# Optimization experiments

Hardware: AMD Instinct MI355X
Metric: run time of the kernel (lower is better)

Reference implementation:

```python
import jax, jax.numpy as jnp
import numpy as np

H, D, TS, A, R, TR = 256, 2, 32, 4, 16, 8  # h_size, max_output_degree, t_size, n_aggr, rank, t_rank
BS = 16384


def setup_inputs() -> dict:
    key = jax.random.key(0)
    ks = jax.random.split(key, 9)
    return {
        "neighbour_h": jax.random.normal(ks[0], (BS, D, H), jnp.float32),
        "type_embs": jax.random.normal(ks[1], (BS, TS), jnp.float32),
        # per-child input projections U: (max_output_degree, n_aggr, h_size, rank)
        "U": jax.random.normal(ks[2], (D, A, H, R), jnp.float32) * 0.05,
        "b": jax.random.normal(ks[3], (D, A, 1, R), jnp.float32) * 0.05,
        # type projection
        "U_type": jax.random.normal(ks[4], (TS, A * TR), jnp.float32) * 0.05,
        "b_type": jax.random.normal(ks[5], (1, A * TR), jnp.float32) * 0.05,
        # stacked augmented core tensors T_list: (n_aggr, t_rank+1, rank+1, rank+1, rank)
        "T": jax.random.normal(ks[6], (A, TR + 1, R + 1, R + 1, R), jnp.float32) * 0.02,
        # output projection
        "U_output": jax.random.normal(ks[7], (A, R, H), jnp.float32) * 0.05,
        "b_output": jax.random.normal(ks[8], (A, 1, H), jnp.float32) * 0.05,
    }


def _aug(x):
    # append a constant-1 feature along the last dim: (bs, a, d) -> (bs, a, d+1)
    bs, a, _ = x.shape
    return jnp.concatenate([x, jnp.ones((bs, a, 1), x.dtype)], axis=-1)


def reference(neighbour_h, type_embs, U, b, U_type, b_type, T, U_output, b_output):
    # child projections: (bs, n_ch, n_aggr, rank)
    ch = jnp.einsum('bch,cahr->bcar', neighbour_h, U) + b[:, :, 0, :]
    # type projection: (bs, n_aggr, t_rank)
    tp = (type_embs @ U_type + b_type).reshape(-1, A, TR)
    # augmented (homogeneous) inputs
    h0 = _aug(tp)         # (bs, a, TR+1)
    h1 = _aug(ch[:, 0])   # (bs, a, R+1)
    h2 = _aug(ch[:, 1])   # (bs, a, R+1)
    # sequential multilinear (Tucker/HOSVD) contraction with the core tensor,
    # vectorized over batch and aggregators (original loops over n_aggr)
    r = jnp.einsum('bap,apqrs->baqrs', h0, T)
    r = jnp.einsum('baq,baqrs->bars', h1, r)
    g = jnp.einsum('bar,bars->bas', h2, r)            # (bs, a, R)
    out = jnp.einsum('bar,arh->bah', g, U_output) + b_output[:, 0, :]
    return out.reshape(neighbour_h.shape[0], -1)      # (bs, n_aggr*h_size)
```

## Files before the change

### kernel.cpp

```cpp
#include <hip/hip_runtime.h>

#define NTHR 512
#define TB 32

typedef __attribute__((ext_vector_type(8))) short bf16x8;
typedef __attribute__((ext_vector_type(16))) float f32x16;
typedef float4 f4;
typedef unsigned short u16;

__device__ __forceinline__ u16 f2b(float x) {
  union { float f; unsigned u; } v; v.f = x;
  unsigned r = (v.u + 0x7fffu + ((v.u >> 16) & 1u)) >> 16;
  return (u16)r;
}
__device__ __forceinline__ float b2f(u16 u) {
  union { unsigned u; float f; } v; v.u = ((unsigned)u) << 16;
  return v.f;
}
__device__ __forceinline__ unsigned pack2(float a, float b) {
  return (unsigned)f2b(a) | ((unsigned)f2b(b) << 16);
}
__device__ __forceinline__ unsigned cvtpk(float lo, float hi) {
  unsigned r;
  asm("v_cvt_pk_bf16_f32 %0, %1, %2" : "=v"(r) : "v"(lo), "v"(hi));
  return r;
}

#define MFMA32(A, B, C) __builtin_amdgcn_mfma_f32_32x32x16_bf16(A, B, C, 0, 0, 0)

extern "C" __global__ void hosvd_prep(const float* __restrict__ U,
                                      const float* __restrict__ T,
                                      const float* __restrict__ UO,
                                      unsigned* __restrict__ ws32) {
  int id = blockIdx.x * 256 + threadIdx.x;
  if (id < 102400) {
    int j2 = id & 3, frag = id >> 2;
    int l = frag & 63, f2 = frag >> 6;
    int nt = f2 % 5, aks = f2 / 5;
    int ks = aks % 20, a = aks / 20;
    int n = nt * 32 + (l & 31);
    int p = n >> 4, s = n & 15;
    float v[2];
    #pragma unroll
    for (int j = 0; j < 2; ++j) {
      int kp = ks * 16 + (l >> 5) * 8 + j2 * 2 + j;
      int q = (unsigned)kp / 18u, r = kp - q * 18;
      float x = 0.f;
      if (p <= 8 && q <= 16 && r <= 16)
        x = T[(((a * 9 + p) * 17 + q) * 17 + r) * 16 + s];
      v[j] = x;
    }
    ws32[id] = pack2(v[0], v[1]);
  } else if (id < 118784) {
    int rel = id - 102400;
    int j2 = rel & 3, frag = rel >> 2;
    int l = frag & 63, f2 = frag >> 6;
    int nt = f2 & 1, ks = (f2 >> 1) & 15, c = f2 >> 5;
    int n = nt * 32 + (l & 31);
    int a = n >> 4, rr = n & 15;
    int k = ks * 16 + (l >> 5) * 8 + j2 * 2;
    float v0 = U[((c * 4 + a) * 256 + k + 0) * 16 + rr];
    float v1 = U[((c * 4 + a) * 256 + k + 1) * 16 + rr];
    ws32[id] = pack2(v0, v1);
  } else if (id < 126976) {
    int rel = id - 118784;
    int j2 = rel & 3, frag = rel >> 2;
    int l = frag & 63, f2 = frag >> 6;
    int ht = f2 & 7, a = f2 >> 3;
    int h = ht * 32 + (l & 31);
    int k = (l >> 5) * 8 + j2 * 2;
    float v0 = UO[(a * 16 + k + 0) * 256 + h];
    float v1 = UO[(a * 16 + k + 1) * 256 + h];
    ws32[id] = pack2(v0, v1);
  }
}

extern "C" __global__ __launch_bounds__(NTHR, 4)
void hosvd_main(const float* __restrict__ nh, const float* __restrict__ te,
                const float* __restrict__ bw, const float* __restrict__ Ut,
                const float* __restrict__ bt, const float* __restrict__ bO,
                const u16* __restrict__ BTf, const u16* __restrict__ UcTf,
                const u16* __restrict__ UOTf, float* __restrict__ out) {
  __shared__ __align__(16) u16   s_u[20800];
  __shared__ __align__(16) u16   s_ch[TB * 164];
  __shared__ __align__(16) float s_tpt[36 * 32];

  const int t = threadIdx.x;
  const int ib0 = blockIdx.x * TB;
  const int w = t >> 6, l = t & 63;
  const int l31 = l & 31, hi = l >> 5;

  float* UtL = (float*)&s_u[16640];
  float* teL = (float*)&s_u[18688];
  float* s_redf = (float*)s_u;

  if (t < 256) {
    const int row = t >> 3, cc = (t >> 2) & 1, aa = t & 3;
    *(uint2*)&s_ch[row * 164 + cc * 80 + aa * 20 + 16] = make_uint2(0x3F80u, 0u);
  }
  if (t < 128) {
    const int aa = t >> 5, row = t & 31;
    s_tpt[(aa * 9 + 8) * 32 + row] = 1.0f;
  }

  if (t < 256) {
    const int row = t >> 3, k4 = t & 7;
    f4 v = *(const f4*)&te[(size_t)(ib0 + row) * 32 + k4 * 4];
    float* d = &teL[row * 33 + k4 * 4];
    d[0] = v.x; d[1] = v.y; d[2] = v.z; d[3] = v.w;
  } else {
    const int j = t - 256;
    *(f4*)&UtL[j * 4] = *(const f4*)&Ut[j * 4];
  }
  for (int lp = t; lp < 4096; lp += NTHR) {
    const int row = lp >> 7, rem = lp & 127;
    const int c = rem >> 6, k0 = (rem & 63) * 4;
    f4 v = *(const f4*)&nh[((size_t)(ib0 + row) * 2 + c) * 256 + k0];
    *(uint2*)&s_u[row * 520 + c * 256 + k0] =
        make_uint2(cvtpk(v.x, v.y), cvtpk(v.z, v.w));
  }
  __syncthreads();

  if (w < 4) {
    const int c = w & 1, nt2 = w >> 1;
    f32x16 accC = {0.f, 0.f, 0.f, 0.f, 0.f, 0.f, 0.f, 0.f,
                   0.f, 0.f, 0.f, 0.f, 0.f, 0.f, 0.f, 0.f};
    #pragma unroll
    for (int ks = 0; ks < 16; ++ks) {
      bf16x8 Av = *(const bf16x8*)&s_u[l31 * 520 + c * 256 + ks * 16 + hi * 8];
      bf16x8 Bv = *(const bf16x8*)
          &UcTf[(size_t)(((c * 16 + ks) * 2 + nt2) * 64 + l) * 8];
      accC = MFMA32(Av, Bv, accC);
    }
    const int n = nt2 * 32 + l31;
    const int ca = n >> 4, rr = n & 15;
    const float bias = bw[(c * 4 + ca) * 16 + rr];
    #pragma unroll
    for (int reg = 0; reg < 16; ++reg) {
      const int row = (reg & 3) + 8 * (reg >> 2) + 4 * hi;
      s_ch[row * 164 + c * 80 + ca * 20 + rr] = f2b(accC[reg] + bias);
    }
  } else {
    const int t2 = t - 256;
    const int i = t2 >> 3, off = (t2 & 7) * 4;
    float ac0 = bt[off], ac1 = bt[off + 1], ac2 = bt[off + 2], ac3 = bt[off + 3];
    #pragma unroll
    for (int k = 0; k < 32; ++k) {
      const float tv = teL[i * 33 + k];
      f4 u = *(const f4*)&UtL[k * 32 + off];
      ac0 = fmaf(tv, u.x, ac0);
      ac1 = fmaf(tv, u.y, ac1);
      ac2 = fmaf(tv, u.z, ac2);
      ac3 = fmaf(tv, u.w, ac3);
    }
    #pragma unroll
    for (int jj = 0; jj < 4; ++jj) {
      const int o2 = off + jj;
      const float v = (jj == 0) ? ac0 : (jj == 1) ? ac1 : (jj == 2) ? ac2 : ac3;
      s_tpt[((o2 >> 3) * 9 + (o2 & 7)) * 32 + i] = v;
    }
  }
  __syncthreads();

  {
    const int a = w & 3, kh = w >> 2;
    const u16* h1g = &s_ch[l31 * 164 + a * 20];
    const u16* h2g = h1g + 80;

    f32x16 acc[5];
    #pragma unroll
    for (int nt = 0; nt < 5; ++nt)
      acc[nt] = (f32x16){0.f, 0.f, 0.f, 0.f, 0.f, 0.f, 0.f, 0.f,
                         0.f, 0.f, 0.f, 0.f, 0.f, 0.f, 0.f, 0.f};

    __builtin_amdgcn_s_setprio(1);
    #pragma unroll
    for (int ks2 = 0; ks2 < 10; ++ks2) {
      const int ks = kh * 10 + ks2;
      const u16* bp = &BTf[(size_t)((a * 20 + ks) * 5) * 512 + l * 8];
      bf16x8 B0 = *(const bf16x8*)(bp + 0 * 512);
      bf16x8 B1 = *(const bf16x8*)(bp + 1 * 512);
      bf16x8 B2 = *(const bf16x8*)(bp + 2 * 512);
      bf16x8 B3 = *(const bf16x8*)(bp + 3 * 512);
      bf16x8 B4 = *(const bf16x8*)(bp + 4 * 512);

      const int k0 = ks * 16 + hi * 8;
      const unsigned q0 = (unsigned)k0 / 18u;
      const int r0 = k0 - (int)q0 * 18;
      const int brk = 18 - r0;
      const float h1a = b2f(h1g[q0]);
      const float h1b = b2f(h1g[q0 + 1]);
      float hv[8];
      #pragma unroll
      for (int j = 0; j < 8; ++j) {
        int rr = r0 + j;
        rr = (rr >= 18) ? rr - 18 : rr;
        const float h2v = b2f(h2g[rr]);
        hv[j] = ((j < brk) ? h1a : h1b) * h2v;
      }
      union { unsigned u[4]; bf16x8 v; } Au;
      Au.u[0] = cvtpk(hv[0], hv[1]);
      Au.u[1] = cvtpk(hv[2], hv[3]);
      Au.u[2] = cvtpk(hv[4], hv[5]);
      Au.u[3] = cvtpk(hv[6], hv[7]);

      acc[0] = MFMA32(Au.v, B0, acc[0]);
      acc[1] = MFMA32(Au.v, B1, acc[1]);
      acc[2] = MFMA32(Au.v, B2, acc[2]);
      acc[3] = MFMA32(Au.v, B3, acc[3]);
      acc[4] = MFMA32(Au.v, B4, acc[4]);
    }
    __builtin_amdgcn_s_setprio(0);

    float gp[16];
    #pragma unroll
    for (int reg = 0; reg < 16; ++reg) gp[reg] = 0.f;
    #pragma unroll
    for (int nt = 0; nt < 5; ++nt) {
      int pp = nt * 2 + (l31 >> 4);
      if (pp > 8) pp = 8;
      const float* tpb = &s_tpt[(a * 9 + pp) * 32 + 4 * hi];
      f4 t0 = *(const f4*)&tpb[0];
      f4 t1 = *(const f4*)&tpb[8];
      f4 t2 = *(const f4*)&tpb[16];
      f4 t3 = *(const f4*)&tpb[24];
      gp[0]  = fmaf(t0.x, acc[nt][0],  gp[0]);
      gp[1]  = fmaf(t0.y, acc[nt][1],  gp[1]);
      gp[2]  = fmaf(t0.z, acc[nt][2],  gp[2]);
      gp[3]  = fmaf(t0.w, acc[nt][3],  gp[3]);
      gp[4]  = fmaf(t1.x, acc[nt][4],  gp[4]);
      gp[5]  = fmaf(t1.y, acc[nt][5],  gp[5]);
      gp[6]  = fmaf(t1.z, acc[nt][6],  gp[6]);
      gp[7]  = fmaf(t1.w, acc[nt][7],  gp[7]);
      gp[8]  = fmaf(t2.x, acc[nt][8],  gp[8]);
      gp[9]  = fmaf(t2.y, acc[nt][9],  gp[9]);
      gp[10] = fmaf(t2.z, acc[nt][10], gp[10]);
      gp[11] = fmaf(t2.w, acc[nt][11], gp[11]);
      gp[12] = fmaf(t3.x, acc[nt][12], gp[12]);
      gp[13] = fmaf(t3.y, acc[nt][13], gp[13]);
      gp[14] = fmaf(t3.z, acc[nt][14], gp[14]);
      gp[15] = fmaf(t3.w, acc[nt][15], gp[15]);
    }
    #pragma unroll
    for (int reg = 0; reg < 16; ++reg)
      gp[reg] += __shfl_xor(gp[reg], 16, 64);
    if ((l & 16) == 0) {
      const int s = l & 15;
      #pragma unroll
      for (int reg = 0; reg < 16; ++reg) {
        const int row = (reg & 3) + 8 * (reg >> 2) + 4 * hi;
        s_redf[((kh * 4 + a) * 32 + row) * 16 + s] = gp[reg];
      }
    }
  }
  __syncthreads();

  {
    #pragma unroll
    for (int a = 0; a < 4; ++a) {
      const float* r0p = &s_redf[((0 + a) * 32 + l31) * 16 + hi * 8];
      const float* r1p = &s_redf[((4 + a) * 32 + l31) * 16 + hi * 8];
      f4 xa = *(const f4*)&r0p[0], xb = *(const f4*)&r0p[4];
      f4 ya = *(const f4*)&r1p[0], yb = *(const f4*)&r1p[4];
      union { unsigned u[4]; bf16x8 v; } Au;
      Au.u[0] = cvtpk(xa.x + ya.x, xa.y + ya.y);
      Au.u[1] = cvtpk(xa.z + ya.z, xa.w + ya.w);
      Au.u[2] = cvtpk(xb.x + yb.x, xb.y + yb.y);
      Au.u[3] = cvtpk(xb.z + yb.z, xb.w + yb.w);
      bf16x8 Bv = *(const bf16x8*)&UOTf[((size_t)(a * 8 + w) * 64 + l) * 8];
      const int h = w * 32 + l31;
      const float bias = bO[a * 256 + h];
      f32x16 accE = {bias, bias, bias, bias, bias, bias, bias, bias,
                     bias, bias, bias, bias, bias, bias, bias, bias};
      accE = MFMA32(Au.v, Bv, accE);
      #pragma unroll
      for (int reg = 0; reg < 16; ++reg) {
        const int row = (reg & 3) + 8 * (reg >> 2) + 4 * hi;
        out[(size_t)(ib0 + row) * 1024 + a * 256 + h] = accE[reg];
      }
    }
  }
}

extern "C" void kernel_launch(void* const* d_in, const int* in_sizes, int n_in,
                              void* d_out, int out_size, void* d_ws, size_t ws_size,
                              hipStream_t stream) {
  const float* nh = (const float*)d_in[0];
  const float* te = (const float*)d_in[1];
  const float* U  = (const float*)d_in[2];
  const float* bw = (const float*)d_in[3];
  const float* Ut = (const float*)d_in[4];
  const float* bt = (const float*)d_in[5];
  const float* T  = (const float*)d_in[6];
  const float* UO = (const float*)d_in[7];
  const float* bO = (const float*)d_in[8];
  float* out = (float*)d_out;

  unsigned* ws32 = (unsigned*)d_ws;
  hipLaunchKernelGGL(hosvd_prep, dim3(496), dim3(256), 0, stream, U, T, UO, ws32);

  const u16* BTf  = (const u16*)d_ws;
  const u16* UcTf = BTf + 204800;
  const u16* UOTf = UcTf + 32768;

  const int bs = in_sizes[0] / 512;
  hipLaunchKernelGGL(hosvd_main, dim3(bs / TB), dim3(NTHR), 0, stream,
                     nh, te, bw, Ut, bt, bO, BTf, UcTf, UOTf, out);
}
```

Baseline: 39.47 us.

## Split fused kernel into projection kernel and per-aggregator contraction kernel

The single fused kernel becomes two. The first computes the child and type projections and writes them to a global workspace. The second runs one small block per (batch tile, aggregator), which gives four times as many blocks, each with less shared memory. The aim is more parallelism and occupancy for the core-tensor MFMA stage, at the cost of an extra launch and a global round trip for the intermediates.

```diff
diff --git a/kernel.cpp b/kernel.cpp
--- a/kernel.cpp
+++ b/kernel.cpp
@@ -1,6 +1,5 @@
 #include <hip/hip_runtime.h>
 
-#define NTHR 512
 #define TB 32
 
 typedef __attribute__((ext_vector_type(8))) short bf16x8;
@@ -75,44 +74,28 @@
   }
 }
 
-extern "C" __global__ __launch_bounds__(NTHR, 4)
-void hosvd_main(const float* __restrict__ nh, const float* __restrict__ te,
-                const float* __restrict__ bw, const float* __restrict__ Ut,
-                const float* __restrict__ bt, const float* __restrict__ bO,
-                const u16* __restrict__ BTf, const u16* __restrict__ UcTf,
-                const u16* __restrict__ UOTf, float* __restrict__ out) {
-  __shared__ __align__(16) u16   s_u[20800];
-  __shared__ __align__(16) u16   s_ch[TB * 164];
-  __shared__ __align__(16) float s_tpt[36 * 32];
+extern "C" __global__ __launch_bounds__(256)
+void hosvd_k1(const float* __restrict__ nh, const float* __restrict__ te,
+              const float* __restrict__ bw, const float* __restrict__ Ut,
+              const float* __restrict__ bt, const u16* __restrict__ UcTf,
+              u16* __restrict__ chg, float* __restrict__ tpg, int bs) {
+  __shared__ __align__(16) u16   s_u[32 * 520];
+  __shared__ __align__(16) float UtL[1024];
+  __shared__ __align__(16) float teL[32 * 33];
 
   const int t = threadIdx.x;
   const int ib0 = blockIdx.x * TB;
   const int w = t >> 6, l = t & 63;
   const int l31 = l & 31, hi = l >> 5;
 
-  float* UtL = (float*)&s_u[16640];
-  float* teL = (float*)&s_u[18688];
-  float* s_redf = (float*)s_u;
-
-  if (t < 256) {
-    const int row = t >> 3, cc = (t >> 2) & 1, aa = t & 3;
-    *(uint2*)&s_ch[row * 164 + cc * 80 + aa * 20 + 16] = make_uint2(0x3F80u, 0u);
-  }
-  if (t < 128) {
-    const int aa = t >> 5, row = t & 31;
-    s_tpt[(aa * 9 + 8) * 32 + row] = 1.0f;
-  }
-
-  if (t < 256) {
+  {
     const int row = t >> 3, k4 = t & 7;
     f4 v = *(const f4*)&te[(size_t)(ib0 + row) * 32 + k4 * 4];
     float* d = &teL[row * 33 + k4 * 4];
     d[0] = v.x; d[1] = v.y; d[2] = v.z; d[3] = v.w;
-  } else {
-    const int j = t - 256;
-    *(f4*)&UtL[j * 4] = *(const f4*)&Ut[j * 4];
-  }
-  for (int lp = t; lp < 4096; lp += NTHR) {
+  }
+  *(f4*)&UtL[t * 4] = *(const f4*)&Ut[t * 4];
+  for (int lp = t; lp < 4096; lp += 256) {
     const int row = lp >> 7, rem = lp & 127;
     const int c = rem >> 6, k0 = (rem & 63) * 4;
     f4 v = *(const f4*)&nh[((size_t)(ib0 + row) * 2 + c) * 256 + k0];
@@ -121,51 +104,100 @@
   }
   __syncthreads();
 
-  if (w < 4) {
-    const int c = w & 1, nt2 = w >> 1;
-    f32x16 accC = {0.f, 0.f, 0.f, 0.f, 0.f, 0.f, 0.f, 0.f,
+  if (w < 2) {
+    const int c = w;
+    f32x16 acc0 = {0.f, 0.f, 0.f, 0.f, 0.f, 0.f, 0.f, 0.f,
                    0.f, 0.f, 0.f, 0.f, 0.f, 0.f, 0.f, 0.f};
+    f32x16 acc1 = acc0;
     #pragma unroll
     for (int ks = 0; ks < 16; ++ks) {
       bf16x8 Av = *(const bf16x8*)&s_u[l31 * 520 + c * 256 + ks * 16 + hi * 8];
-      bf16x8 Bv = *(const bf16x8*)
-          &UcTf[(size_t)(((c * 16 + ks) * 2 + nt2) * 64 + l) * 8];
-      accC = MFMA32(Av, Bv, accC);
-    }
-    const int n = nt2 * 32 + l31;
-    const int ca = n >> 4, rr = n & 15;
-    const float bias = bw[(c * 4 + ca) * 16 + rr];
+      bf16x8 B0 = *(const bf16x8*)&UcTf[(size_t)(((c * 16 + ks) * 2 + 0) * 64 + l) * 8];
+      bf16x8 B1 = *(const bf16x8*)&UcTf[(size_t)(((c * 16 + ks) * 2 + 1) * 64 + l) * 8];
+      acc0 = MFMA32(Av, B0, acc0);
+      acc1 = MFMA32(Av, B1, acc1);
+    }
+    const int rr = l31 & 15;
+    const int ca0 = l31 >> 4;
+    const int ca1 = 2 + (l31 >> 4);
+    const float b0 = bw[(c * 4 + ca0) * 16 + rr];
+    const float b1 = bw[(c * 4 + ca1) * 16 + rr];
     #pragma unroll
     for (int reg = 0; reg < 16; ++reg) {
       const int row = (reg & 3) + 8 * (reg >> 2) + 4 * hi;
-      s_ch[row * 164 + c * 80 + ca * 20 + rr] = f2b(accC[reg] + bias);
+      const size_t base = (size_t)(ib0 + row) * 160;
+      chg[base + ca0 * 40 + c * 20 + rr] = f2b(acc0[reg] + b0);
+      chg[base + ca1 * 40 + c * 20 + rr] = f2b(acc1[reg] + b1);
+    }
+    #pragma unroll
+    for (int u2 = 0; u2 < 2; ++u2) {
+      const int unit = l + u2 * 64;
+      const int item = unit & 31, aa = unit >> 5;
+      *(uint2*)&chg[(size_t)(ib0 + item) * 160 + aa * 40 + c * 20 + 16] =
+          make_uint2(0x3F80u, 0u);
     }
   } else {
-    const int t2 = t - 256;
-    const int i = t2 >> 3, off = (t2 & 7) * 4;
-    float ac0 = bt[off], ac1 = bt[off + 1], ac2 = bt[off + 2], ac3 = bt[off + 3];
+    const int t2 = t - 128;
+    const int i = t2 >> 2, a = t2 & 3;
+    float acc[8];
+    #pragma unroll
+    for (int p = 0; p < 8; ++p) acc[p] = bt[a * 8 + p];
     #pragma unroll
     for (int k = 0; k < 32; ++k) {
       const float tv = teL[i * 33 + k];
-      f4 u = *(const f4*)&UtL[k * 32 + off];
-      ac0 = fmaf(tv, u.x, ac0);
-      ac1 = fmaf(tv, u.y, ac1);
-      ac2 = fmaf(tv, u.z, ac2);
-      ac3 = fmaf(tv, u.w, ac3);
-    }
-    #pragma unroll
-    for (int jj = 0; jj < 4; ++jj) {
-      const int o2 = off + jj;
-      const float v = (jj == 0) ? ac0 : (jj == 1) ? ac1 : (jj == 2) ? ac2 : ac3;
-      s_tpt[((o2 >> 3) * 9 + (o2 & 7)) * 32 + i] = v;
-    }
+      f4 u0 = *(const f4*)&UtL[k * 32 + a * 8];
+      f4 u1 = *(const f4*)&UtL[k * 32 + a * 8 + 4];
+      acc[0] = fmaf(tv, u0.x, acc[0]);
+      acc[1] = fmaf(tv, u0.y, acc[1]);
+      acc[2] = fmaf(tv, u0.z, acc[2]);
+      acc[3] = fmaf(tv, u0.w, acc[3]);
+      acc[4] = fmaf(tv, u1.x, acc[4]);
+      acc[5] = fmaf(tv, u1.y, acc[5]);
+      acc[6] = fmaf(tv, u1.z, acc[6]);
+      acc[7] = fmaf(tv, u1.w, acc[7]);
+    }
+    #pragma unroll
+    for (int p = 0; p < 8; ++p)
+      tpg[(size_t)(a * 12 + p) * bs + ib0 + i] = acc[p];
+    tpg[(size_t)(a * 12 + 8) * bs + ib0 + i] = 1.0f;
+  }
+}
+
+extern "C" __global__ __launch_bounds__(128, 4)
+void hosvd_k2(const u16* __restrict__ chg, const float* __restrict__ tpg,
+              const float* __restrict__ bO, const u16* __restrict__ BTf,
+              const u16* __restrict__ UOTf, float* __restrict__ out, int bs) {
+  __shared__ __align__(16) u16   s_ch[32 * 44];
+  __shared__ __align__(16) float s_tpt[9 * 32];
+  __shared__ __align__(16) float s_red[2 * 32 * 16];
+
+  const int t = threadIdx.x;
+  const int a = blockIdx.x & 3;
+  const int ib0 = (blockIdx.x >> 2) * TB;
+  const int l = t & 63;
+  const int l31 = l & 31, hi = l >> 5;
+  const int kh = t >> 6;
+
+  {
+    const int item = t & 31, grp = t >> 5;
+    const unsigned* src =
+        (const unsigned*)chg + ((size_t)(ib0 + item) * 80 + a * 20 + grp * 5);
+    unsigned v0 = src[0], v1 = src[1], v2 = src[2], v3 = src[3], v4 = src[4];
+    unsigned* dst = (unsigned*)s_ch + item * 22 +
+                    ((grp < 2) ? grp * 5 : 11 + (grp - 2) * 5);
+    dst[0] = v0; dst[1] = v1; dst[2] = v2; dst[3] = v3; dst[4] = v4;
+  }
+  {
+    const int li = t & 31;
+    for (int pp = t >> 5; pp < 9; pp += 4)
+      s_tpt[pp * 32 + li] = tpg[(size_t)(a * 12 + pp) * bs + ib0 + li];
   }
   __syncthreads();
 
   {
-    const int a = w & 3, kh = w >> 2;
-    const u16* h1g = &s_ch[l31 * 164 + a * 20];
-    const u16* h2g = h1g + 80;
+    const u16* h1g = &s_ch[l31 * 44];
+    const u16* h2g = h1g + 22;
+    const u16* bbase = &BTf[(size_t)((a * 20 + kh * 10) * 5) * 512 + l * 8];
 
     f32x16 acc[5];
     #pragma unroll
@@ -176,14 +208,14 @@
     __builtin_amdgcn_s_setprio(1);
     #pragma unroll
     for (int ks2 = 0; ks2 < 10; ++ks2) {
-      const int ks = kh * 10 + ks2;
-      const u16* bp = &BTf[(size_t)((a * 20 + ks) * 5) * 512 + l * 8];
+      const u16* bp = bbase + ks2 * 2560;
       bf16x8 B0 = *(const bf16x8*)(bp + 0 * 512);
       bf16x8 B1 = *(const bf16x8*)(bp + 1 * 512);
       bf16x8 B2 = *(const bf16x8*)(bp + 2 * 512);
       bf16x8 B3 = *(const bf16x8*)(bp + 3 * 512);
       bf16x8 B4 = *(const bf16x8*)(bp + 4 * 512);
 
+      const int ks = kh * 10 + ks2;
       const int k0 = ks * 16 + hi * 8;
       const unsigned q0 = (unsigned)k0 / 18u;
       const int r0 = k0 - (int)q0 * 18;
@@ -219,7 +251,7 @@
     for (int nt = 0; nt < 5; ++nt) {
       int pp = nt * 2 + (l31 >> 4);
       if (pp > 8) pp = 8;
-      const float* tpb = &s_tpt[(a * 9 + pp) * 32 + 4 * hi];
+      const float* tpb = &s_tpt[pp * 32 + 4 * hi];
       f4 t0 = *(const f4*)&tpb[0];
       f4 t1 = *(const f4*)&tpb[8];
       f4 t2 = *(const f4*)&tpb[16];
@@ -249,34 +281,34 @@
       #pragma unroll
       for (int reg = 0; reg < 16; ++reg) {
         const int row = (reg & 3) + 8 * (reg >> 2) + 4 * hi;
-        s_redf[((kh * 4 + a) * 32 + row) * 16 + s] = gp[reg];
+        s_red[(kh * 32 + row) * 16 + s] = gp[reg];
       }
     }
   }
   __syncthreads();
 
   {
-    #pragma unroll
-    for (int a = 0; a < 4; ++a) {
-      const float* r0p = &s_redf[((0 + a) * 32 + l31) * 16 + hi * 8];
-      const float* r1p = &s_redf[((4 + a) * 32 + l31) * 16 + hi * 8];
-      f4 xa = *(const f4*)&r0p[0], xb = *(const f4*)&r0p[4];
-      f4 ya = *(const f4*)&r1p[0], yb = *(const f4*)&r1p[4];
-      union { unsigned u[4]; bf16x8 v; } Au;
-      Au.u[0] = cvtpk(xa.x + ya.x, xa.y + ya.y);
-      Au.u[1] = cvtpk(xa.z + ya.z, xa.w + ya.w);
-      Au.u[2] = cvtpk(xb.x + yb.x, xb.y + yb.y);
-      Au.u[3] = cvtpk(xb.z + yb.z, xb.w + yb.w);
-      bf16x8 Bv = *(const bf16x8*)&UOTf[((size_t)(a * 8 + w) * 64 + l) * 8];
-      const int h = w * 32 + l31;
-      const float bias = bO[a * 256 + h];
+    const float* r0p = &s_red[l31 * 16 + hi * 8];
+    const float* r1p = &s_red[(32 + l31) * 16 + hi * 8];
+    f4 xa = *(const f4*)&r0p[0], xb = *(const f4*)&r0p[4];
+    f4 ya = *(const f4*)&r1p[0], yb = *(const f4*)&r1p[4];
+    union { unsigned u[4]; bf16x8 v; } Au;
+    Au.u[0] = cvtpk(xa.x + ya.x, xa.y + ya.y);
+    Au.u[1] = cvtpk(xa.z + ya.z, xa.w + ya.w);
+    Au.u[2] = cvtpk(xb.x + yb.x, xb.y + yb.y);
+    Au.u[3] = cvtpk(xb.z + yb.z, xb.w + yb.w);
+    #pragma unroll
+    for (int j = 0; j < 4; ++j) {
+      const int ht = kh * 4 + j;
+      bf16x8 Bv = *(const bf16x8*)&UOTf[((size_t)(a * 8 + ht) * 64 + l) * 8];
+      const float bias = bO[a * 256 + ht * 32 + l31];
       f32x16 accE = {bias, bias, bias, bias, bias, bias, bias, bias,
                      bias, bias, bias, bias, bias, bias, bias, bias};
       accE = MFMA32(Au.v, Bv, accE);
       #pragma unroll
       for (int reg = 0; reg < 16; ++reg) {
         const int row = (reg & 3) + 8 * (reg >> 2) + 4 * hi;
-        out[(size_t)(ib0 + row) * 1024 + a * 256 + h] = accE[reg];
+        out[(size_t)(ib0 + row) * 1024 + a * 256 + ht * 32 + l31] = accE[reg];
       }
     }
   }
@@ -302,8 +334,12 @@
   const u16* BTf  = (const u16*)d_ws;
   const u16* UcTf = BTf + 204800;
   const u16* UOTf = UcTf + 32768;
+  u16*   chg = (u16*)((char*)d_ws + 524288);
+  float* tpg = (float*)((char*)d_ws + 524288 + 5242880);
 
   const int bs = in_sizes[0] / 512;
-  hipLaunchKernelGGL(hosvd_main, dim3(bs / TB), dim3(NTHR), 0, stream,
-                     nh, te, bw, Ut, bt, bO, BTf, UcTf, UOTf, out);
-}
+  hipLaunchKernelGGL(hosvd_k1, dim3(bs / TB), dim3(256), 0, stream,
+                     nh, te, bw, Ut, bt, UcTf, chg, tpg, bs);
+  hipLaunchKernelGGL(hosvd_k2, dim3((bs / TB) * 4), dim3(128), 0, stream,
+                     chg, tpg, bO, BTf, UOTf, out, bs);
+}
```

New measurement: 44.95 us. 1.14x slower.
